# Kernel tuning notes

Hardware: AMD Instinct MI355X
Metric: run time of the kernel (lower is better)

## Reference

```python
import jax, jax.numpy as jnp
import numpy as np

D_MODEL = 384
HEAD_SIZE = 64
CONTEXT = 100


def setup_inputs() -> dict:
    key = jax.random.key(0)
    kx, kq, kk, kv = jax.random.split(key, 4)
    x = jax.random.normal(kx, (1024, CONTEXT, D_MODEL), dtype=jnp.float32)
    s = 1.0 / np.sqrt(D_MODEL)
    Wq = jax.random.normal(kq, (D_MODEL, HEAD_SIZE), dtype=jnp.float32) * s
    Wk = jax.random.normal(kk, (D_MODEL, HEAD_SIZE), dtype=jnp.float32) * s
    Wv = jax.random.normal(kv, (D_MODEL, HEAD_SIZE), dtype=jnp.float32) * s
    return {"x": x, "Wq": Wq, "Wk": Wk, "Wv": Wv}


def reference(x, Wq, Wk, Wv):
    B, T, C = x.shape
    q = jnp.einsum('btc,ch->bth', x, Wq)
    k = jnp.einsum('btc,ch->bth', x, Wk)
    v = jnp.einsum('btc,ch->bth', x, Wv)
    # Faithful to source bug: divide by d**(-0.5) == multiply by sqrt(d)
    scale = jnp.asarray(k.shape[-1], x.dtype) ** 0.5
    wei = jnp.einsum('bth,bsh->bts', q, k) * scale  # [B,T,T]
    causal = jnp.tril(jnp.ones((T, T), dtype=bool))
    wei = jnp.where(causal, wei, -jnp.inf)
    wei = jax.nn.softmax(wei, axis=-1)
    # dropout: eval mode (identity)
    return jnp.einsum('bts,bsh->bth', wei, v)
```

## Files before the change

### kernel.cpp

```cpp
#include <hip/hip_runtime.h>
#include <hip/hip_fp16.h>

#define T_CTX 100
#define C_DIM 384
#define H_DIM 64

typedef _Float16 half8   __attribute__((ext_vector_type(8)));
typedef _Float16 half2_t __attribute__((ext_vector_type(2)));
typedef float    f32x4   __attribute__((ext_vector_type(4)));

#define QH_OFF 0
#define QL_OFF 7168
#define KH_OFF 14336
#define KL_OFF 21504
#define VT_OFF 28672
#define PS_OFF 0
#define SMEM_BYTES 73728
#define XS_STRIDE_F 36
#define XS_BUF_F 4608

__global__ void prep_w_kernel(const float* __restrict__ Wq,
                              const float* __restrict__ Wk,
                              const float* __restrict__ Wv,
                              _Float16* __restrict__ wf_hi,
                              _Float16* __restrict__ wf_lo) {
    int idx = blockIdx.x * 256 + threadIdx.x;
    if (idx >= 9216) return;
    int lane  = idx & 63;
    int chunk = (idx >> 6) % 12;
    int jt    = idx / (64 * 12);
    int col   = jt * 16 + (lane & 15);
    const float* W = (col < 64) ? Wq : ((col < 128) ? Wk : Wv);
    int h = col & 63;
    int cbase = chunk * 32 + (lane >> 4) * 8;
    #pragma unroll
    for (int e = 0; e < 8; ++e) {
        float f = W[(size_t)(cbase + e) * H_DIM + h];
        _Float16 hi = (_Float16)f;
        _Float16 lo = (_Float16)(f - (float)hi);
        size_t o = (size_t)idx * 8 + e;
        wf_hi[o] = hi;
        wf_lo[o] = lo;
    }
}

__device__ inline void cvt_hilo(f32x4 a, f32x4 c, half8& hh, half8& ll) {
    float f[8] = {a[0], a[1], a[2], a[3], c[0], c[1], c[2], c[3]};
    #pragma unroll
    for (int u = 0; u < 8; ++u) {
        _Float16 h = (_Float16)f[u];
        hh[u] = h;
        ll[u] = (_Float16)(f[u] - (float)h);
    }
}

__global__ __launch_bounds__(512, 4)
void head_kernel(const float* __restrict__ x,
                 const _Float16* __restrict__ wf_hi,
                 const _Float16* __restrict__ wf_lo,
                 float* __restrict__ out) {
    extern __shared__ _Float16 sm[];
    float* xsf = (float*)sm;

    const int b    = blockIdx.x;
    const int tid  = threadIdx.x;
    const int lane = tid & 63;
    const int wid  = tid >> 6;
    const int l15  = lane & 15;
    const int lg   = lane >> 4;
    const int mh   = wid >> 2;
    const int nw   = wid & 3;
    const int NI   = (mh == 0) ? 4 : 3;
    const bool isK = (nw >= 2);

    int t0, t1, t2, t3;
    if (!isK) { t0 = nw * 2; t1 = t0 + 1; t2 = 8 + nw * 2; t3 = t2 + 1; }
    else      { t0 = 4 + (nw - 2) * 2; t1 = t0 + 1; t2 = t0; t3 = t1; }

    const float* xb = x + (size_t)b * T_CTX * C_DIM;

    const int r0 = tid >> 3, r1 = r0 + 64, c4 = tid & 7;

    f32x4 acc0[4], acc1[4], acc2[4], acc3[4];
    #pragma unroll
    for (int i = 0; i < 4; ++i) {
        acc0[i] = (f32x4){0.f,0.f,0.f,0.f};
        acc1[i] = (f32x4){0.f,0.f,0.f,0.f};
        acc2[i] = (f32x4){0.f,0.f,0.f,0.f};
        acc3[i] = (f32x4){0.f,0.f,0.f,0.f};
    }

    {
        f32x4 va = (r0 < T_CTX) ? *(const f32x4*)(xb + (size_t)r0 * C_DIM + c4 * 4)
                                : (f32x4){0.f,0.f,0.f,0.f};
        f32x4 vb = (r1 < T_CTX) ? *(const f32x4*)(xb + (size_t)r1 * C_DIM + c4 * 4)
                                : (f32x4){0.f,0.f,0.f,0.f};
        *(f32x4*)(xsf + r0 * XS_STRIDE_F + c4 * 4) = va;
        *(f32x4*)(xsf + r1 * XS_STRIDE_F + c4 * 4) = vb;
    }
    __syncthreads();

    #pragma unroll 1
    for (int kc = 0; kc < 12; ++kc) {
        const int nk = kc + 1;
        f32x4 lda = (f32x4){0.f,0.f,0.f,0.f}, ldb = (f32x4){0.f,0.f,0.f,0.f};
        if (nk < 12) {
            if (r0 < T_CTX) lda = *(const f32x4*)(xb + (size_t)r0 * C_DIM + nk * 32 + c4 * 4);
            if (r1 < T_CTX) ldb = *(const f32x4*)(xb + (size_t)r1 * C_DIM + nk * 32 + c4 * 4);
        }
        const float* xc = xsf + (kc & 1) * XS_BUF_F;

        const size_t wo0 = ((size_t)(t0 * 12 + kc) * 64 + lane) * 8;
        const size_t wo1 = ((size_t)(t1 * 12 + kc) * 64 + lane) * 8;
        half8 B0 = *(const half8*)(wf_hi + wo0);
        half8 B1 = *(const half8*)(wf_hi + wo1);
        half8 B2, B3;
        if (!isK) {
            B2 = *(const half8*)(wf_hi + ((size_t)(t2 * 12 + kc) * 64 + lane) * 8);
            B3 = *(const half8*)(wf_hi + ((size_t)(t3 * 12 + kc) * 64 + lane) * 8);
        } else {
            B2 = *(const half8*)(wf_lo + wo0);
            B3 = *(const half8*)(wf_lo + wo1);
        }

        #pragma unroll
        for (int i = 0; i < 4; ++i) {
            if (i >= NI) break;
            int row = mh * 64 + i * 16 + l15;
            const float* p = xc + row * XS_STRIDE_F + lg * 8;
            f32x4 xa = *(const f32x4*)p;
            f32x4 xv = *(const f32x4*)(p + 4);
            half8 ah, al;
            cvt_hilo(xa, xv, ah, al);
            acc0[i] = __builtin_amdgcn_mfma_f32_16x16x32_f16(ah, B0, acc0[i], 0, 0, 0);
            acc0[i] = __builtin_amdgcn_mfma_f32_16x16x32_f16(al, B0, acc0[i], 0, 0, 0);
            acc1[i] = __builtin_amdgcn_mfma_f32_16x16x32_f16(ah, B1, acc1[i], 0, 0, 0);
            acc1[i] = __builtin_amdgcn_mfma_f32_16x16x32_f16(al, B1, acc1[i], 0, 0, 0);
            if (!isK) {
                acc2[i] = __builtin_amdgcn_mfma_f32_16x16x32_f16(ah, B2, acc2[i], 0, 0, 0);
                acc3[i] = __builtin_amdgcn_mfma_f32_16x16x32_f16(ah, B3, acc3[i], 0, 0, 0);
            } else {
                acc0[i] = __builtin_amdgcn_mfma_f32_16x16x32_f16(ah, B2, acc0[i], 0, 0, 0);
                acc1[i] = __builtin_amdgcn_mfma_f32_16x16x32_f16(ah, B3, acc1[i], 0, 0, 0);
            }
        }

        if (nk < 12) {
            float* xn = xsf + (nk & 1) * XS_BUF_F;
            *(f32x4*)(xn + r0 * XS_STRIDE_F + c4 * 4) = lda;
            *(f32x4*)(xn + r1 * XS_STRIDE_F + c4 * 4) = ldb;
        }
        __syncthreads();
    }

    {
        int jh = tid >> 7;
        int w2 = (tid & 127) * 2;
        *(half2_t*)(sm + VT_OFF + jh * 2048 + 1792 + w2) =
            (half2_t){(_Float16)0.f, (_Float16)0.f};
    }

    #pragma unroll
    for (int i = 0; i < 4; ++i) {
        if (i >= NI) break;
        #pragma unroll
        for (int r = 0; r < 4; ++r) {
            int row = mh * 64 + i * 16 + lg * 4 + r;
            if (!isK) {
                {
                    int h = t0 * 16 + l15;
                    int off = (row >> 4) * 1024 + (h >> 5) * 512
                            + (((h >> 3) & 3) * 16 + (row & 15)) * 8 + (h & 7);
                    float v0 = acc0[i][r];
                    _Float16 hh = (_Float16)v0;
                    sm[QH_OFF + off] = hh;
                    sm[QL_OFF + off] = (_Float16)(v0 - (float)hh);
                }
                {
                    int h = t1 * 16 + l15;
                    int off = (row >> 4) * 1024 + (h >> 5) * 512
                            + (((h >> 3) & 3) * 16 + (row & 15)) * 8 + (h & 7);
                    float v0 = acc1[i][r];
                    _Float16 hh = (_Float16)v0;
                    sm[QH_OFF + off] = hh;
                    sm[QL_OFF + off] = (_Float16)(v0 - (float)hh);
                }
                {
                    int h = (t2 - 8) * 16 + l15;
                    int off = (h >> 4) * 2048 + (row >> 5) * 512
                            + (((row >> 3) & 3) * 16 + (h & 15)) * 8 + (row & 7);
                    sm[VT_OFF + off] = (_Float16)acc2[i][r];
                }
                {
                    int h = (t3 - 8) * 16 + l15;
                    int off = (h >> 4) * 2048 + (row >> 5) * 512
                            + (((row >> 3) & 3) * 16 + (h & 15)) * 8 + (row & 7);
                    sm[VT_OFF + off] = (_Float16)acc3[i][r];
                }
            } else {
                {
                    int h = (t0 - 4) * 16 + l15;
                    int off = (row >> 4) * 1024 + (h >> 5) * 512
                            + (((h >> 3) & 3) * 16 + (row & 15)) * 8 + (h & 7);
                    float v0 = acc0[i][r];
                    _Float16 hh = (_Float16)v0;
                    sm[KH_OFF + off] = hh;
                    sm[KL_OFF + off] = (_Float16)(v0 - (float)hh);
                }
                {
                    int h = (t1 - 4) * 16 + l15;
                    int off = (row >> 4) * 1024 + (h >> 5) * 512
                            + (((h >> 3) & 3) * 16 + (row & 15)) * 8 + (h & 7);
                    float v0 = acc1[i][r];
                    _Float16 hh = (_Float16)v0;
                    sm[KH_OFF + off] = hh;
                    sm[KL_OFF + off] = (_Float16)(v0 - (float)hh);
                }
            }
        }
    }
    __syncthreads();

    f32x4 sacc[7];
    float rsum[4] = {0.f, 0.f, 0.f, 0.f};

    if (wid < 7) {
        #pragma unroll
        for (int j = 0; j < 7; ++j) sacc[j] = (f32x4){0.f,0.f,0.f,0.f};
        #pragma unroll
        for (int kk = 0; kk < 2; ++kk) {
            half8 qh = *(const half8*)(sm + QH_OFF + wid * 1024 + kk * 512 + lane * 8);
            half8 ql = *(const half8*)(sm + QL_OFF + wid * 1024 + kk * 512 + lane * 8);
            #pragma unroll
            for (int j = 0; j < 7; ++j) {
                half8 kh = *(const half8*)(sm + KH_OFF + j * 1024 + kk * 512 + lane * 8);
                half8 kl = *(const half8*)(sm + KL_OFF + j * 1024 + kk * 512 + lane * 8);
                sacc[j] = __builtin_amdgcn_mfma_f32_16x16x32_f16(qh, kh, sacc[j], 0, 0, 0);
                sacc[j] = __builtin_amdgcn_mfma_f32_16x16x32_f16(ql, kh, sacc[j], 0, 0, 0);
                sacc[j] = __builtin_amdgcn_mfma_f32_16x16x32_f16(qh, kl, sacc[j], 0, 0, 0);
            }
        }
        float rmax[4] = {-1e30f, -1e30f, -1e30f, -1e30f};
        #pragma unroll
        for (int j = 0; j < 7; ++j) {
            int key = j * 16 + l15;
            #pragma unroll
            for (int r = 0; r < 4; ++r) {
                int row = wid * 16 + lg * 4 + r;
                float s = (key <= row && key < T_CTX) ? sacc[j][r] * 8.0f : -1e30f;
                sacc[j][r] = s;
                rmax[r] = fmaxf(rmax[r], s);
            }
        }
        #pragma unroll
        for (int r = 0; r < 4; ++r) {
            #pragma unroll
            for (int d = 1; d < 16; d <<= 1)
                rmax[r] = fmaxf(rmax[r], __shfl_xor(rmax[r], d, 64));
            rsum[r] = rmax[r];
        }
    }
    __syncthreads();

    if (wid < 7) {
        float rmax[4];
        #pragma unroll
        for (int r = 0; r < 4; ++r) { rmax[r] = rsum[r]; rsum[r] = 0.f; }
        #pragma unroll
        for (int j = 0; j < 7; ++j) {
            int key = j * 16 + l15;
            #pragma unroll
            for (int r = 0; r < 4; ++r) {
                float p = __expf(sacc[j][r] - rmax[r]);
                rsum[r] += p;
                int a = lg * 4 + r;
                int off = wid * 2048 + (key >> 5) * 512
                        + (((key >> 3) & 3) * 16 + a) * 8 + (key & 7);
                sm[PS_OFF + off] = (_Float16)p;
            }
        }
        #pragma unroll
        for (int r = 0; r < 4; ++r) {
            int key = 112 + l15;
            int a = lg * 4 + r;
            int off = wid * 2048 + (key >> 5) * 512
                    + (((key >> 3) & 3) * 16 + a) * 8 + (key & 7);
            sm[PS_OFF + off] = (_Float16)0.f;
            #pragma unroll
            for (int d = 1; d < 16; d <<= 1)
                rsum[r] += __shfl_xor(rsum[r], d, 64);
        }
    }
    __syncthreads();

    if (wid < 7) {
        f32x4 oacc[4];
        #pragma unroll
        for (int j = 0; j < 4; ++j) oacc[j] = (f32x4){0.f,0.f,0.f,0.f};
        #pragma unroll
        for (int kk = 0; kk < 4; ++kk) {
            half8 pa = *(const half8*)(sm + PS_OFF + wid * 2048 + kk * 512 + lane * 8);
            #pragma unroll
            for (int jh = 0; jh < 4; ++jh) {
                half8 vb = *(const half8*)(sm + VT_OFF + jh * 2048 + kk * 512 + lane * 8);
                oacc[jh] = __builtin_amdgcn_mfma_f32_16x16x32_f16(pa, vb, oacc[jh], 0, 0, 0);
            }
        }
        float rinv[4];
        #pragma unroll
        for (int r = 0; r < 4; ++r) rinv[r] = 1.0f / rsum[r];
        #pragma unroll
        for (int jh = 0; jh < 4; ++jh) {
            #pragma unroll
            for (int r = 0; r < 4; ++r) {
                int t = wid * 16 + lg * 4 + r;
                if (t < T_CTX)
                    out[((size_t)b * T_CTX + t) * H_DIM + jh * 16 + l15] = oacc[jh][r] * rinv[r];
            }
        }
    }
}

extern "C" void kernel_launch(void* const* d_in, const int* in_sizes, int n_in,
                              void* d_out, int out_size, void* d_ws, size_t ws_size,
                              hipStream_t stream) {
    const float* x  = (const float*)d_in[0];
    const float* Wq = (const float*)d_in[1];
    const float* Wk = (const float*)d_in[2];
    const float* Wv = (const float*)d_in[3];

    _Float16* wf_hi = (_Float16*)d_ws;
    _Float16* wf_lo = wf_hi + (size_t)9216 * 8;

    prep_w_kernel<<<36, 256, 0, stream>>>(Wq, Wk, Wv, wf_hi, wf_lo);

    (void)hipFuncSetAttribute((const void*)head_kernel,
                              hipFuncAttributeMaxDynamicSharedMemorySize, SMEM_BYTES);
    head_kernel<<<1024, 512, SMEM_BYTES, stream>>>(x, wf_hi, wf_lo, (float*)d_out);
}
```

Measured before the change: 75.18 us.

## Convert x to fp16 hi/lo once at staging and prefetch weight fragments

```diff
diff --git a/kernel.cpp b/kernel.cpp
--- a/kernel.cpp
+++ b/kernel.cpp
@@ -6,6 +6,7 @@
 #define H_DIM 64
 
 typedef _Float16 half8   __attribute__((ext_vector_type(8)));
+typedef _Float16 half4_t __attribute__((ext_vector_type(4)));
 typedef _Float16 half2_t __attribute__((ext_vector_type(2)));
 typedef float    f32x4   __attribute__((ext_vector_type(4)));
 
@@ -16,8 +17,6 @@
 #define VT_OFF 28672
 #define PS_OFF 0
 #define SMEM_BYTES 73728
-#define XS_STRIDE_F 36
-#define XS_BUF_F 4608
 
 __global__ void prep_w_kernel(const float* __restrict__ Wq,
                               const float* __restrict__ Wk,
@@ -44,13 +43,12 @@
     }
 }
 
-__device__ inline void cvt_hilo(f32x4 a, f32x4 c, half8& hh, half8& ll) {
-    float f[8] = {a[0], a[1], a[2], a[3], c[0], c[1], c[2], c[3]};
-    #pragma unroll
-    for (int u = 0; u < 8; ++u) {
-        _Float16 h = (_Float16)f[u];
+__device__ inline void cvt4(f32x4 v, half4_t& hh, half4_t& ll) {
+    #pragma unroll
+    for (int u = 0; u < 4; ++u) {
+        _Float16 h = (_Float16)v[u];
         hh[u] = h;
-        ll[u] = (_Float16)(f[u] - (float)h);
+        ll[u] = (_Float16)(v[u] - (float)h);
     }
 }
 
@@ -60,7 +58,6 @@
                  const _Float16* __restrict__ wf_lo,
                  float* __restrict__ out) {
     extern __shared__ _Float16 sm[];
-    float* xsf = (float*)sm;
 
     const int b    = blockIdx.x;
     const int tid  = threadIdx.x;
@@ -73,13 +70,23 @@
     const int NI   = (mh == 0) ? 4 : 3;
     const bool isK = (nw >= 2);
 
-    int t0, t1, t2, t3;
-    if (!isK) { t0 = nw * 2; t1 = t0 + 1; t2 = 8 + nw * 2; t3 = t2 + 1; }
-    else      { t0 = 4 + (nw - 2) * 2; t1 = t0 + 1; t2 = t0; t3 = t1; }
+    int t0, t1;
+    const _Float16 *pw0, *pw1, *pw2, *pw3;
+    if (!isK) {
+        t0 = nw * 2; t1 = t0 + 1;
+        pw0 = wf_hi + (size_t)t0 * 6144;
+        pw1 = wf_hi + (size_t)t1 * 6144;
+        pw2 = wf_hi + (size_t)(8 + nw * 2) * 6144;
+        pw3 = wf_hi + (size_t)(9 + nw * 2) * 6144;
+    } else {
+        t0 = 4 + (nw - 2) * 2; t1 = t0 + 1;
+        pw0 = wf_hi + (size_t)t0 * 6144;
+        pw1 = wf_hi + (size_t)t1 * 6144;
+        pw2 = wf_lo + (size_t)t0 * 6144;
+        pw3 = wf_lo + (size_t)t1 * 6144;
+    }
 
     const float* xb = x + (size_t)b * T_CTX * C_DIM;
-
-    const int r0 = tid >> 3, r1 = r0 + 64, c4 = tid & 7;
 
     f32x4 acc0[4], acc1[4], acc2[4], acc3[4];
     #pragma unroll
@@ -90,67 +97,85 @@
         acc3[i] = (f32x4){0.f,0.f,0.f,0.f};
     }
 
-    {
-        f32x4 va = (r0 < T_CTX) ? *(const f32x4*)(xb + (size_t)r0 * C_DIM + c4 * 4)
-                                : (f32x4){0.f,0.f,0.f,0.f};
-        f32x4 vb = (r1 < T_CTX) ? *(const f32x4*)(xb + (size_t)r1 * C_DIM + c4 * 4)
-                                : (f32x4){0.f,0.f,0.f,0.f};
-        *(f32x4*)(xsf + r0 * XS_STRIDE_F + c4 * 4) = va;
-        *(f32x4*)(xsf + r1 * XS_STRIDE_F + c4 * 4) = vb;
-    }
+    #pragma unroll
+    for (int s = 0; s < 2; ++s) {
+        int f4  = tid + s * 512;
+        int row = f4 >> 3;
+        int c4  = f4 & 7;
+        f32x4 v = (f32x4){0.f, 0.f, 0.f, 0.f};
+        if (row < T_CTX) v = *(const f32x4*)(xb + (size_t)row * C_DIM + c4 * 4);
+        half4_t hh, ll;
+        cvt4(v, hh, ll);
+        int o = row * 40 + c4 * 4;
+        *(half4_t*)(sm + o)        = hh;
+        *(half4_t*)(sm + 5120 + o) = ll;
+    }
+    half8 W0 = *(const half8*)(pw0 + lane * 8);
+    half8 W1 = *(const half8*)(pw1 + lane * 8);
+    half8 W2 = *(const half8*)(pw2 + lane * 8);
+    half8 W3 = *(const half8*)(pw3 + lane * 8);
     __syncthreads();
 
     #pragma unroll 1
     for (int kc = 0; kc < 12; ++kc) {
         const int nk = kc + 1;
-        f32x4 lda = (f32x4){0.f,0.f,0.f,0.f}, ldb = (f32x4){0.f,0.f,0.f,0.f};
+        f32x4 ld[2];
+        half8 N0 = W0, N1 = W1, N2 = W2, N3 = W3;
         if (nk < 12) {
-            if (r0 < T_CTX) lda = *(const f32x4*)(xb + (size_t)r0 * C_DIM + nk * 32 + c4 * 4);
-            if (r1 < T_CTX) ldb = *(const f32x4*)(xb + (size_t)r1 * C_DIM + nk * 32 + c4 * 4);
-        }
-        const float* xc = xsf + (kc & 1) * XS_BUF_F;
-
-        const size_t wo0 = ((size_t)(t0 * 12 + kc) * 64 + lane) * 8;
-        const size_t wo1 = ((size_t)(t1 * 12 + kc) * 64 + lane) * 8;
-        half8 B0 = *(const half8*)(wf_hi + wo0);
-        half8 B1 = *(const half8*)(wf_hi + wo1);
-        half8 B2, B3;
-        if (!isK) {
-            B2 = *(const half8*)(wf_hi + ((size_t)(t2 * 12 + kc) * 64 + lane) * 8);
-            B3 = *(const half8*)(wf_hi + ((size_t)(t3 * 12 + kc) * 64 + lane) * 8);
-        } else {
-            B2 = *(const half8*)(wf_lo + wo0);
-            B3 = *(const half8*)(wf_lo + wo1);
-        }
-
+            #pragma unroll
+            for (int s = 0; s < 2; ++s) {
+                int f4  = tid + s * 512;
+                int row = f4 >> 3;
+                int c4  = f4 & 7;
+                ld[s] = (f32x4){0.f, 0.f, 0.f, 0.f};
+                if (row < T_CTX)
+                    ld[s] = *(const f32x4*)(xb + (size_t)row * C_DIM + nk * 32 + c4 * 4);
+            }
+            const int wo = nk * 512 + lane * 8;
+            N0 = *(const half8*)(pw0 + wo);
+            N1 = *(const half8*)(pw1 + wo);
+            N2 = *(const half8*)(pw2 + wo);
+            N3 = *(const half8*)(pw3 + wo);
+        }
+
+        const _Float16* xh = sm + (kc & 1) * 10240;
+        const _Float16* xl = xh + 5120;
         #pragma unroll
         for (int i = 0; i < 4; ++i) {
             if (i >= NI) break;
             int row = mh * 64 + i * 16 + l15;
-            const float* p = xc + row * XS_STRIDE_F + lg * 8;
-            f32x4 xa = *(const f32x4*)p;
-            f32x4 xv = *(const f32x4*)(p + 4);
-            half8 ah, al;
-            cvt_hilo(xa, xv, ah, al);
-            acc0[i] = __builtin_amdgcn_mfma_f32_16x16x32_f16(ah, B0, acc0[i], 0, 0, 0);
-            acc0[i] = __builtin_amdgcn_mfma_f32_16x16x32_f16(al, B0, acc0[i], 0, 0, 0);
-            acc1[i] = __builtin_amdgcn_mfma_f32_16x16x32_f16(ah, B1, acc1[i], 0, 0, 0);
-            acc1[i] = __builtin_amdgcn_mfma_f32_16x16x32_f16(al, B1, acc1[i], 0, 0, 0);
+            int o = row * 40 + lg * 8;
+            half8 ah = *(const half8*)(xh + o);
+            half8 al = *(const half8*)(xl + o);
+            acc0[i] = __builtin_amdgcn_mfma_f32_16x16x32_f16(ah, W0, acc0[i], 0, 0, 0);
+            acc0[i] = __builtin_amdgcn_mfma_f32_16x16x32_f16(al, W0, acc0[i], 0, 0, 0);
+            acc1[i] = __builtin_amdgcn_mfma_f32_16x16x32_f16(ah, W1, acc1[i], 0, 0, 0);
+            acc1[i] = __builtin_amdgcn_mfma_f32_16x16x32_f16(al, W1, acc1[i], 0, 0, 0);
             if (!isK) {
-                acc2[i] = __builtin_amdgcn_mfma_f32_16x16x32_f16(ah, B2, acc2[i], 0, 0, 0);
-                acc3[i] = __builtin_amdgcn_mfma_f32_16x16x32_f16(ah, B3, acc3[i], 0, 0, 0);
+                acc2[i] = __builtin_amdgcn_mfma_f32_16x16x32_f16(ah, W2, acc2[i], 0, 0, 0);
+                acc3[i] = __builtin_amdgcn_mfma_f32_16x16x32_f16(ah, W3, acc3[i], 0, 0, 0);
             } else {
-                acc0[i] = __builtin_amdgcn_mfma_f32_16x16x32_f16(ah, B2, acc0[i], 0, 0, 0);
-                acc1[i] = __builtin_amdgcn_mfma_f32_16x16x32_f16(ah, B3, acc1[i], 0, 0, 0);
+                acc0[i] = __builtin_amdgcn_mfma_f32_16x16x32_f16(ah, W2, acc0[i], 0, 0, 0);
+                acc1[i] = __builtin_amdgcn_mfma_f32_16x16x32_f16(ah, W3, acc1[i], 0, 0, 0);
             }
         }
 
         if (nk < 12) {
-            float* xn = xsf + (nk & 1) * XS_BUF_F;
-            *(f32x4*)(xn + r0 * XS_STRIDE_F + c4 * 4) = lda;
-            *(f32x4*)(xn + r1 * XS_STRIDE_F + c4 * 4) = ldb;
+            const int nb = (nk & 1) * 10240;
+            #pragma unroll
+            for (int s = 0; s < 2; ++s) {
+                int f4  = tid + s * 512;
+                int row = f4 >> 3;
+                int c4  = f4 & 7;
+                half4_t hh, ll;
+                cvt4(ld[s], hh, ll);
+                int o = row * 40 + c4 * 4;
+                *(half4_t*)(sm + nb + o)        = hh;
+                *(half4_t*)(sm + nb + 5120 + o) = ll;
+            }
         }
         __syncthreads();
+        W0 = N0; W1 = N1; W2 = N2; W3 = N3;
     }
 
     {
@@ -186,13 +211,13 @@
                     sm[QL_OFF + off] = (_Float16)(v0 - (float)hh);
                 }
                 {
-                    int h = (t2 - 8) * 16 + l15;
+                    int h = nw * 32 + l15;
                     int off = (h >> 4) * 2048 + (row >> 5) * 512
                             + (((row >> 3) & 3) * 16 + (h & 15)) * 8 + (row & 7);
                     sm[VT_OFF + off] = (_Float16)acc2[i][r];
                 }
                 {
-                    int h = (t3 - 8) * 16 + l15;
+                    int h = nw * 32 + 16 + l15;
                     int off = (h >> 4) * 2048 + (row >> 5) * 512
                             + (((row >> 3) & 3) * 16 + (h & 15)) * 8 + (row & 7);
                     sm[VT_OFF + off] = (_Float16)acc3[i][r];
```

Measured after the change: 64.17 us, median of 2. -14.6%, faster.
